# Kernel optimization log

Hardware: AMD Instinct MI355X
Metric: run time of the kernel (lower is better)

## Reference

```python
import jax, jax.numpy as jnp
import numpy as np

B, D = 64, 65536   # batch, num default boxes
NEG_POS = 3        # negative:positive mining ratio (init arg)


def _bce_with_logits(x, t):
    # numerically stable elementwise BCE-with-logits (matches torch)
    return jnp.maximum(x, 0.0) - x * t + jnp.log1p(jnp.exp(-jnp.abs(x)))


def _smooth_l1(d):
    ad = jnp.abs(d)
    return jnp.where(ad < 1.0, 0.5 * d * d, ad - 0.5)


def setup_inputs() -> dict:
    key = jax.random.key(0)
    k1, k2, k3, k4 = jax.random.split(key, 4)
    loc_data = jax.random.normal(k1, (B, D, 4), dtype=jnp.float32)
    conf_data = jax.random.normal(k2, (B, D, 1), dtype=jnp.float32)
    loc_t = jax.random.normal(k3, (B, D, 4), dtype=jnp.float32)
    conf_t = (jax.random.uniform(k4, (B, D)) < 0.02).astype(jnp.int32)
    return {"loc_data": loc_data, "conf_data": conf_data,
            "loc_t": loc_t, "conf_t": conf_t}


def reference(loc_data, conf_data, loc_t, conf_t):
    pos = conf_t > 0                                  # [B, D]
    num_pos = pos.sum(axis=1, keepdims=True)          # [B, 1]

    # ---- localization loss: smooth-L1 mean over positive box coords ----
    pf = pos[:, :, None].astype(loc_data.dtype)       # [B, D, 1]
    sl1 = _smooth_l1(loc_data - loc_t) * pf           # [B, D, 4]
    n_loc_elems = pf.sum() * 4.0                      # masked-gather -> mean
    loss_l = sl1.sum() / n_loc_elems

    # ---- confidence loss with hard negative mining ----
    logits = conf_data[:, :, 0]                       # [B, D]
    bce = _bce_with_logits(logits, conf_t.astype(logits.dtype))
    bce_neg = jnp.where(pos, 0.0, bce)                # zero-out positives
    # double argsort -> per-row rank of each element's loss (descending)
    loss_idx = jnp.argsort(-bce_neg, axis=1)          # [B, D]
    idx_rank = jnp.argsort(loss_idx, axis=1)          # [B, D]
    num_neg = jnp.minimum(num_pos * NEG_POS, D)       # [B, 1]
    neg = idx_rank < num_neg                          # top-k hardest negatives
    sel = (pos | neg).astype(logits.dtype)            # [B, D]
    loss_c = (bce * sel).sum() / sel.sum()            # mean over selected

    N = num_pos.sum().astype(logits.dtype)
    return (loss_l / N, loss_c / N)
```

## Files before the change

kernel.cpp:

```cpp
#include <hip/hip_runtime.h>
#include <stdint.h>


#define B_ 64
#define D_ 65536
#define NEGPOS 3
#define BPR 16
#define NBLK (B_ * BPR)
#define CHUNK (D_ / BPR)
#define XC 1.25f
#define CAPC 16384
#define NREG 32

#define OFF_SL1P     0
#define OFF_BCEP     8192
#define OFF_NP       16384
#define OFF_CC       20480
#define OFF_NEGSUM   24576
#define OFF_KSEL     25088
#define OFF_CAND     32768

__device__ __forceinline__ float softplus_f(float x) {
    return fmaxf(x, 0.0f) + log1pf(expf(-fabsf(x)));
}

__device__ __forceinline__ unsigned sortkey(float x) {
    unsigned u = __float_as_uint(x);
    return (u & 0x80000000u) ? ~u : (u | 0x80000000u);
}
__device__ __forceinline__ float unsortkey(unsigned s) {
    unsigned u = (s & 0x80000000u) ? (s & 0x7FFFFFFFu) : ~s;
    return __uint_as_float(u);
}

__device__ __forceinline__ float smooth_l1_4(float4 a, float4 b) {
    float s = 0.0f, d, ad;
    d = a.x - b.x; ad = fabsf(d); s += (ad < 1.0f) ? 0.5f * d * d : ad - 0.5f;
    d = a.y - b.y; ad = fabsf(d); s += (ad < 1.0f) ? 0.5f * d * d : ad - 0.5f;
    d = a.z - b.z; ad = fabsf(d); s += (ad < 1.0f) ? 0.5f * d * d : ad - 0.5f;
    d = a.w - b.w; ad = fabsf(d); s += (ad < 1.0f) ? 0.5f * d * d : ad - 0.5f;
    return s;
}

__device__ __forceinline__ double wredD(double v) {
#pragma unroll
    for (int o = 32; o > 0; o >>= 1) v += __shfl_down(v, o, 64);
    return v;
}
__device__ __forceinline__ int wredI(int v) {
#pragma unroll
    for (int o = 32; o > 0; o >>= 1) v += __shfl_down(v, o, 64);
    return v;
}

__global__ void __launch_bounds__(256)
mbl_k1(const float4* __restrict__ loc4, const float* __restrict__ conf,
       const float4* __restrict__ loct4, const int* __restrict__ conft,
       unsigned char* __restrict__ ws)
{
    __shared__ float lcand[CHUNK];
    __shared__ unsigned short lpos[CHUNK];
    __shared__ unsigned wtot[4];
    __shared__ double wr[8];

    const int block = blockIdx.x;
    const int base = block * CHUNK;
    const float4* c4 = (const float4*)(conf + base);
    const int4*   t4 = (const int4*)(conft + base);
    const int lane = threadIdx.x & 63, wid = threadIdx.x >> 6;

    float4 xv[4]; int4 tv[4];
#pragma unroll
    for (int it = 0; it < 4; it++) {
        const int g = threadIdx.x + it * 256;
        xv[it] = c4[g];
        tv[it] = t4[g];
    }

    double bcep = 0.0;
    unsigned cntc = 0, cntp = 0;
#pragma unroll
    for (int it = 0; it < 4; it++) {
#pragma unroll
        for (int c = 0; c < 4; c++) {
            float x = (c == 0) ? xv[it].x : (c == 1) ? xv[it].y : (c == 2) ? xv[it].z : xv[it].w;
            int   t = (c == 0) ? tv[it].x : (c == 1) ? tv[it].y : (c == 2) ? tv[it].z : tv[it].w;
            if (t > 0) { cntp++; bcep += (double)(softplus_f(x) - x); }
            else if (x >= XC) cntc++;
        }
    }

    unsigned pk = (cntc << 16) | cntp;
    unsigned incl = pk;
#pragma unroll
    for (int o = 1; o < 64; o <<= 1) {
        unsigned v = __shfl_up(incl, o, 64);
        if (lane >= o) incl += v;
    }
    unsigned excl = incl - pk;
    if (lane == 63) wtot[wid] = incl;
    __syncthreads();
    unsigned wbase = 0;
    for (int w = 0; w < wid; w++) wbase += wtot[w];
    const unsigned tot = wtot[0] + wtot[1] + wtot[2] + wtot[3];
    const unsigned totc = tot >> 16, totp = tot & 0xFFFFu;
    unsigned offc = (excl >> 16) + (wbase >> 16);
    unsigned offp = (excl & 0xFFFFu) + (wbase & 0xFFFFu);

#pragma unroll
    for (int it = 0; it < 4; it++) {
#pragma unroll
        for (int c = 0; c < 4; c++) {
            float x = (c == 0) ? xv[it].x : (c == 1) ? xv[it].y : (c == 2) ? xv[it].z : xv[it].w;
            int   t = (c == 0) ? tv[it].x : (c == 1) ? tv[it].y : (c == 2) ? tv[it].z : tv[it].w;
            const int li = (threadIdx.x + it * 256) * 4 + c;
            if (t > 0) lpos[offp++] = (unsigned short)li;
            else if (x >= XC) lcand[offc++] = x;
        }
    }
    __syncthreads();

    float* seg = (float*)(ws + OFF_CAND) + (size_t)block * CHUNK;
    for (unsigned i = threadIdx.x; i < totc; i += 256) seg[i] = lcand[i];

    double sl1 = 0.0;
    for (unsigned i = threadIdx.x; i < totp; i += 256) {
        const int e = base + (int)lpos[i];
        sl1 += (double)smooth_l1_4(loc4[e], loct4[e]);
    }

    double s1 = wredD(sl1), s2 = wredD(bcep);
    if (lane == 0) { wr[wid] = s1; wr[4 + wid] = s2; }
    __syncthreads();
    if (threadIdx.x == 0) {
        ((double*)(ws + OFF_SL1P))[block] = wr[0] + wr[1] + wr[2] + wr[3];
        ((double*)(ws + OFF_BCEP))[block] = wr[4] + wr[5] + wr[6] + wr[7];
        ((unsigned*)(ws + OFF_NP))[block] = totp;
        ((unsigned*)(ws + OFF_CC))[block] = totc;
    }
}

__device__ __forceinline__ int blockSumI(int v, int* sh) {
    int w = wredI(v);
    const int lane = threadIdx.x & 63, wid = threadIdx.x >> 6;
    __syncthreads();
    if (lane == 0) sh[wid] = w;
    __syncthreads();
    return sh[0] + sh[1] + sh[2] + sh[3];
}

__global__ void __launch_bounds__(256)
mbl_ksel(const float* __restrict__ conf, const int* __restrict__ conft,
         unsigned char* __restrict__ ws)
{
    __shared__ unsigned segoff[BPR + 1];
    __shared__ int shI[4];
    __shared__ double wr[4];

    const int row = blockIdx.x;
    const unsigned* cc = (const unsigned*)(ws + OFF_CC) + row * BPR;
    const unsigned* npb = (const unsigned*)(ws + OFF_NP) + row * BPR;

    if (threadIdx.x == 0) {
        unsigned o = 0;
        int np = 0;
#pragma unroll
        for (int s = 0; s < BPR; s++) { segoff[s] = o; o += cc[s]; np += (int)npb[s]; }
        segoff[BPR] = o;
        shI[0] = np;
    }
    __syncthreads();
    const int np = shI[0];
    const unsigned n = segoff[BPR];
    long long k = (long long)np * NEGPOS;
    if (k > D_) k = D_;
    long long negs = (long long)D_ - np;
    if (k > negs) k = negs;
    if (threadIdx.x == 0) ((int*)(ws + OFF_KSEL))[row] = (int)k;
    if (k <= 0) {
        if (threadIdx.x == 0) ((double*)(ws + OFF_NEGSUM))[row] = 0.0;
        return;
    }
    __syncthreads();

    const bool fb = ((long long)n < k) || (n > (unsigned)(NREG * 256)) ||
                    (n > (unsigned)CAPC);
    const float* cand = (const float*)(ws + OFF_CAND);
    const float* rowc = conf + row * D_;
    const int*   rowt = conft + row * D_;
    const int lane = threadIdx.x & 63, wid = threadIdx.x >> 6;
    unsigned lo = 0u, hi = 0xFFFFFFFFu;
    int rem;
    unsigned Tkey;

    if (!fb) {
        unsigned keys[NREG];
#pragma unroll
        for (int j = 0; j < NREG; j++) {
            const unsigned g = (unsigned)(j * 256) + threadIdx.x;
            unsigned key = 0u;
            if (g < n) {
                int s = 0;
#pragma unroll
                for (int st = 8; st > 0; st >>= 1)
                    if (s + st <= BPR && segoff[s + st] <= g) s += st;
                const unsigned idx = g - segoff[s];
                key = sortkey(cand[(size_t)(row * BPR + s) * CHUNK + idx]);
            }
            keys[j] = key;
        }
        for (int it = 0; it < 32; it++) {
            const unsigned mid = lo + ((hi - lo) >> 1);
            int c = 0;
#pragma unroll
            for (int j = 0; j < NREG; j++) c += (keys[j] > mid) ? 1 : 0;
            const int tot = blockSumI(c, shI);
            if ((long long)tot >= k) lo = mid; else hi = mid;
        }
        Tkey = hi;
        int c = 0;
#pragma unroll
        for (int j = 0; j < NREG; j++) c += (keys[j] > Tkey) ? 1 : 0;
        rem = (int)(k - (long long)blockSumI(c, shI));

        double acc = 0.0;
#pragma unroll
        for (int j = 0; j < NREG; j++)
            if (keys[j] > Tkey) acc += (double)softplus_f(unsortkey(keys[j]));
        double t = wredD(acc);
        if (lane == 0) wr[wid] = t;
        __syncthreads();
        if (threadIdx.x == 0)
            ((double*)(ws + OFF_NEGSUM))[row] =
                wr[0] + wr[1] + wr[2] + wr[3] +
                (double)rem * (double)softplus_f(unsortkey(Tkey));
    } else {
        for (int it = 0; it < 32; it++) {
            const unsigned mid = lo + ((hi - lo) >> 1);
            int c = 0;
            for (int i = threadIdx.x; i < D_; i += 256)
                if (rowt[i] <= 0 && sortkey(rowc[i]) > mid) c++;
            const int tot = blockSumI(c, shI);
            if ((long long)tot >= k) lo = mid; else hi = mid;
        }
        Tkey = hi;
        int c = 0;
        double acc = 0.0;
        for (int i = threadIdx.x; i < D_; i += 256) {
            if (rowt[i] <= 0) {
                float x = rowc[i];
                if (sortkey(x) > Tkey) { c++; acc += (double)softplus_f(x); }
            }
        }
        rem = (int)(k - (long long)blockSumI(c, shI));
        double t = wredD(acc);
        if (lane == 0) wr[wid] = t;
        __syncthreads();
        if (threadIdx.x == 0)
            ((double*)(ws + OFF_NEGSUM))[row] =
                wr[0] + wr[1] + wr[2] + wr[3] +
                (double)rem * (double)softplus_f(unsortkey(Tkey));
    }
}

__global__ void __launch_bounds__(256)
mbl_k5(unsigned char* __restrict__ ws, float* __restrict__ out)
{
    __shared__ double wrA[4], wrB[4], wrC[4];
    __shared__ int shN[4], shK[4];
    const double* sl1p = (const double*)(ws + OFF_SL1P);
    const double* bcep = (const double*)(ws + OFF_BCEP);
    const unsigned* npb = (const unsigned*)(ws + OFF_NP);
    const int* ksel = (const int*)(ws + OFF_KSEL);
    const double* ns = (const double*)(ws + OFF_NEGSUM);

    double a = 0.0, b = 0.0, c = 0.0;
    int n = 0, kk = 0;
    for (int i = threadIdx.x; i < NBLK; i += 256) {
        a += sl1p[i]; b += bcep[i]; n += (int)npb[i];
    }
    if (threadIdx.x < 64) { kk = ksel[threadIdx.x]; c = ns[threadIdx.x]; }

    double ra = wredD(a), rb = wredD(b), rc = wredD(c);
    int rn = wredI(n), rk = wredI(kk);
    const int lane = threadIdx.x & 63, wid = threadIdx.x >> 6;
    if (lane == 0) { wrA[wid] = ra; wrB[wid] = rb; wrC[wid] = rc; shN[wid] = rn; shK[wid] = rk; }
    __syncthreads();
    if (threadIdx.x == 0) {
        double SL1 = wrA[0] + wrA[1] + wrA[2] + wrA[3];
        double BCE = wrB[0] + wrB[1] + wrB[2] + wrB[3];
        double NSUM = wrC[0] + wrC[1] + wrC[2] + wrC[3];
        double Np = (double)(shN[0] + shN[1] + shN[2] + shN[3]);
        double Kt = (double)(shK[0] + shK[1] + shK[2] + shK[3]);
        double out0 = (Np > 0.0) ? (SL1 / (4.0 * Np)) / Np : 0.0;
        double denom = Np + Kt;
        double out1 = (Np > 0.0 && denom > 0.0) ? ((BCE + NSUM) / denom) / Np : 0.0;
        out[0] = (float)out0;
        out[1] = (float)out1;
    }
}

extern "C" void kernel_launch(void* const* d_in, const int* in_sizes, int n_in,
                              void* d_out, int out_size, void* d_ws, size_t ws_size,
                              hipStream_t stream)
{
    const float4* loc4  = (const float4*)d_in[0];
    const float*  conf  = (const float*)d_in[1];
    const float4* loct4 = (const float4*)d_in[2];
    const int*    conft = (const int*)d_in[3];
    unsigned char* ws = (unsigned char*)d_ws;
    float* out = (float*)d_out;

    mbl_k1<<<dim3(NBLK), dim3(256), 0, stream>>>(loc4, conf, loct4, conft, ws);
    mbl_ksel<<<dim3(B_), dim3(256), 0, stream>>>(conf, conft, ws);
    mbl_k5<<<dim3(1), dim3(256), 0, stream>>>(ws, out);
}
```

Measured before the change: 195.4 us.

## Replace 32-step radix bisection with histogram plus in-bin rank selection for top-k threshold

The per-row k-th largest threshold search over candidate negatives used 32 rounds of block-wide bisection, each ending in a block reduction with barriers. It is replaced by a 4096-bin shared-memory histogram over the candidate values, a serial scan to find the bin holding the k-th element, and an exact O(c^2) rank selection inside that bin. Bisection is kept as a fallback when the bin overflows its buffer. This cuts barrier and reduction rounds but adds shared-memory atomics, a single-thread scan and larger shared-memory use, which may lower occupancy.

```diff
diff --git a/kernel.cpp b/kernel.cpp
--- a/kernel.cpp
+++ b/kernel.cpp
@@ -11,6 +11,9 @@
 #define XC 1.25f
 #define CAPC 16384
 #define NREG 32
+#define HBINS 4096
+#define XRANGE 5.0f
+#define CJCAP 1024
 
 #define OFF_SL1P     0
 #define OFF_BCEP     8192
@@ -31,6 +34,11 @@
 __device__ __forceinline__ float unsortkey(unsigned s) {
     unsigned u = (s & 0x80000000u) ? (s & 0x7FFFFFFFu) : ~s;
     return __uint_as_float(u);
+}
+
+__device__ __forceinline__ int bin_of_x(float x) {
+    int b = (int)((x - XC) * ((float)HBINS / XRANGE));
+    return max(0, min(HBINS - 1, b));
 }
 
 __device__ __forceinline__ float smooth_l1_4(float4 a, float4 b) {
@@ -154,6 +162,10 @@
          unsigned char* __restrict__ ws)
 {
     __shared__ unsigned segoff[BPR + 1];
+    __shared__ unsigned hist[HBINS];
+    __shared__ unsigned part[256];
+    __shared__ unsigned ubuf[CJCAP];
+    __shared__ unsigned shJ, shRemJ, shCj, shT;
     __shared__ int shI[4];
     __shared__ double wr[4];
 
@@ -189,9 +201,8 @@
     const float* rowc = conf + row * D_;
     const int*   rowt = conft + row * D_;
     const int lane = threadIdx.x & 63, wid = threadIdx.x >> 6;
-    unsigned lo = 0u, hi = 0xFFFFFFFFu;
+    unsigned Tkey;
     int rem;
-    unsigned Tkey;
 
     if (!fb) {
         unsigned keys[NREG];
@@ -209,24 +220,86 @@
             }
             keys[j] = key;
         }
-        for (int it = 0; it < 32; it++) {
-            const unsigned mid = lo + ((hi - lo) >> 1);
-            int c = 0;
-#pragma unroll
-            for (int j = 0; j < NREG; j++) c += (keys[j] > mid) ? 1 : 0;
-            const int tot = blockSumI(c, shI);
-            if ((long long)tot >= k) lo = mid; else hi = mid;
-        }
-        Tkey = hi;
+
+        for (int i = threadIdx.x; i < HBINS; i += 256) hist[i] = 0;
+        __syncthreads();
+#pragma unroll
+        for (int j = 0; j < NREG; j++)
+            if (keys[j]) atomicAdd(&hist[bin_of_x(unsortkey(keys[j]))], 1u);
+        __syncthreads();
+
+        {
+            unsigned s = 0; const int b0 = threadIdx.x * 16;
+#pragma unroll
+            for (int i = 0; i < 16; i++) s += hist[b0 + i];
+            part[threadIdx.x] = s;
+        }
+        __syncthreads();
+        if (threadIdx.x == 0) {
+            long long cum = 0; unsigned J = 0, remJ = 0;
+            for (int t = 255; t >= 0; t--) {
+                if (cum + (long long)part[t] >= k) {
+                    for (int b = t * 16 + 15; b >= t * 16; b--) {
+                        cum += hist[b];
+                        if (cum >= k) {
+                            J = (unsigned)b;
+                            remJ = (unsigned)(k - (cum - (long long)hist[b]));
+                            break;
+                        }
+                    }
+                    break;
+                }
+                cum += part[t];
+            }
+            shJ = J; shRemJ = remJ; shCj = 0;
+        }
+        __syncthreads();
+        const unsigned J = shJ, remJ = shRemJ;
+
+#pragma unroll
+        for (int j = 0; j < NREG; j++) {
+            if (keys[j] && (unsigned)bin_of_x(unsortkey(keys[j])) == J) {
+                unsigned p = atomicAdd(&shCj, 1u);
+                if (p < CJCAP) ubuf[p] = keys[j];
+            }
+        }
+        __syncthreads();
+        const unsigned cj = shCj;
+
+        if (cj <= CJCAP) {
+            for (unsigned i = threadIdx.x; i < cj; i += 256) {
+                const unsigned ki = ubuf[i];
+                unsigned gt = 0, ge = 0;
+                for (unsigned l = 0; l < cj; l++) {
+                    const unsigned kl = ubuf[l];
+                    gt += (kl > ki) ? 1u : 0u;
+                    ge += (kl >= ki) ? 1u : 0u;
+                }
+                if (gt < remJ && ge >= remJ) shT = ki;
+            }
+            __syncthreads();
+            Tkey = shT;
+        } else {
+            unsigned lo = 0u, hi = 0xFFFFFFFFu;
+            for (int it = 0; it < 32; it++) {
+                const unsigned mid = lo + ((hi - lo) >> 1);
+                int c = 0;
+#pragma unroll
+                for (int j = 0; j < NREG; j++) c += (keys[j] > mid) ? 1 : 0;
+                const int tot = blockSumI(c, shI);
+                if ((long long)tot >= k) lo = mid; else hi = mid;
+            }
+            Tkey = hi;
+        }
+
         int c = 0;
-#pragma unroll
-        for (int j = 0; j < NREG; j++) c += (keys[j] > Tkey) ? 1 : 0;
-        rem = (int)(k - (long long)blockSumI(c, shI));
-
         double acc = 0.0;
 #pragma unroll
-        for (int j = 0; j < NREG; j++)
-            if (keys[j] > Tkey) acc += (double)softplus_f(unsortkey(keys[j]));
+        for (int j = 0; j < NREG; j++) {
+            if (keys[j] > Tkey) { c++; acc += (double)softplus_f(unsortkey(keys[j])); }
+        }
+        const int tot = blockSumI(c, shI);
+        rem = (int)(k - (long long)tot);
         double t = wredD(acc);
         if (lane == 0) wr[wid] = t;
         __syncthreads();
@@ -235,6 +308,7 @@
                 wr[0] + wr[1] + wr[2] + wr[3] +
                 (double)rem * (double)softplus_f(unsortkey(Tkey));
     } else {
+        unsigned lo = 0u, hi = 0xFFFFFFFFu;
         for (int it = 0; it < 32; it++) {
             const unsigned mid = lo + ((hi - lo) >> 1);
             int c = 0;
```

Measured after the change: 195.2 us. Within noise of the previous version (-0.1%).
